# Kernel optimization log

Hardware: AMD Instinct MI355X
Metric: run time of the kernel (lower is better)

Reference implementation:

```python
import jax, jax.numpy as jnp
import numpy as np

N = 100000
D = 128       # out_feats
QK = 32       # qk_dim
E = 1600000
K_HOPS = 7    # self._k


def setup_inputs() -> dict:
    key = jax.random.key(0)
    ks = jax.random.split(key, 10)
    h_train = jax.random.normal(ks[0], (N, D), dtype=jnp.float32)
    h_ori = jax.random.normal(ks[1], (N, D), dtype=jnp.float32)
    edge_index = jax.random.randint(ks[2], (2, E), 0, N, dtype=jnp.int64)
    s = 1.0 / np.sqrt(D)
    Wq = jax.random.uniform(ks[3], (D, QK), jnp.float32, -s, s)
    bq = jnp.zeros((QK,), jnp.float32)
    Wk = jax.random.uniform(ks[4], (D, QK), jnp.float32, -s, s)
    bk = jnp.zeros((QK,), jnp.float32)
    Wv = jax.random.uniform(ks[5], (D, D), jnp.float32, -s, s)
    bv = jnp.zeros((D,), jnp.float32)
    return {"h_train": h_train, "h_ori": h_ori, "edge_index": edge_index,
            "Wq": Wq, "bq": bq, "Wk": Wk, "bk": bk, "Wv": Wv, "bv": bv}


def _propagate(x, D_invsqrt, row, col):
    h = x * D_invsqrt
    m = h[row]                                   # [E, D] gather
    out = jax.ops.segment_sum(m, col, num_segments=N)
    return out * D_invsqrt


def reference(h_train, h_ori, edge_index, Wq, bq, Wk, bk, Wv, bv):
    x = h_train
    row, col = edge_index[0], edge_index[1]
    deg = jax.ops.segment_sum(jnp.ones((E,), x.dtype), row, num_segments=N)
    deg = jnp.clip(deg, 1.0)
    D_invsqrt = (deg ** -0.5)[:, None]           # [N,1]

    a_feat = x + _propagate(x, D_invsqrt, row, col)
    stack = [a_feat]
    for _ in range(K_HOPS):
        # unnLaplacian high pass: x - Ax_hat (dropout inactive in eval)
        x = x - _propagate(x, D_invsqrt, row, col)
        stack.append(x)
    L_stack = jnp.stack(stack, axis=1)           # [N, K, D]

    # FullAttention with global mean query
    q = h_ori @ Wq + bq                          # [N, QK]
    q_global = q.mean(axis=0)                    # [QK]
    keys = L_stack @ Wk + bk                     # [N, K, QK]
    values = L_stack @ Wv + bv                   # [N, K, D]
    scale = 1.0 / np.sqrt(D)                     # D = keys input last dim
    scores = jnp.einsum('q,nkq->nk', q_global, keys) * scale
    A = jax.nn.softmax(scores, axis=-1)          # [N, K]
    V = jnp.einsum('nk,nkd->nd', A, values)      # [N, D] (== sum over K dim)
    return V
```

## Files before the change

### kernel.cpp

```cpp
#include <hip/hip_runtime.h>
#include <hip/hip_fp16.h>
#include <math.h>

#define DFEAT 128
#define QKD 32
#define NPART 512

typedef _Float16 half8 __attribute__((ext_vector_type(8)));
typedef float floatx4 __attribute__((ext_vector_type(4)));

static inline size_t align256(size_t x) { return (x + 255) & ~size_t(255); }


__global__ void count_row_kernel(const int* __restrict__ eidx, unsigned* __restrict__ cnt_row, int E) {
    int e = blockIdx.x * blockDim.x + threadIdx.x;
    if (e < E) atomicAdd(&cnt_row[eidx[e]], 1u);
}

__global__ void dinv_kernel(const unsigned* __restrict__ cnt_row, float* __restrict__ dinv,
                            float* __restrict__ dinv2, float* __restrict__ rec, int n) {
    int i = blockIdx.x * blockDim.x + threadIdx.x;
    if (i < n) {
        unsigned c = cnt_row[i];
        if (c < 1u) c = 1u;
        float fd = (float)c;
        float sq = sqrtf(fd);
        dinv[i] = 1.0f / sq;
        dinv2[i] = 1.0f / fd;
        rec[i] = sq;
    }
}


__global__ void __launch_bounds__(1024)
hist_kernel(const int* __restrict__ eidx, unsigned* __restrict__ bcount, int E, int nbuk) {
    __shared__ unsigned h[512];
    for (int i = threadIdx.x; i < 512; i += 1024) h[i] = 0;
    __syncthreads();
    int base = blockIdx.x * 8192;
    int end = base + 8192; if (end > E) end = E;
    for (int i = base + threadIdx.x; i < end; i += 1024)
        atomicAdd(&h[(unsigned)eidx[E + i] >> 8], 1u);
    __syncthreads();
    for (int i = threadIdx.x; i < nbuk; i += 1024)
        if (h[i]) atomicAdd(&bcount[i], h[i]);
}


__global__ void bscan_kernel(const unsigned* __restrict__ bcount, unsigned* __restrict__ bbase,
                             unsigned* __restrict__ bcur, unsigned* __restrict__ colptr,
                             int nbuk, int n, int E) {
    __shared__ unsigned s[512];
    int t = threadIdx.x;
    unsigned v = (t < nbuk) ? bcount[t] : 0u;
    s[t] = v; __syncthreads();
    for (int off = 1; off < 512; off <<= 1) {
        unsigned u = (t >= off) ? s[t - off] : 0u;
        __syncthreads();
        s[t] += u;
        __syncthreads();
    }
    if (t < nbuk) { unsigned e = s[t] - v; bbase[t] = e; bcur[t] = e; }
    if (t == 0) { bbase[nbuk] = (unsigned)E; colptr[n] = (unsigned)E; }
}

__global__ void __launch_bounds__(1024)
bscatter_kernel(const int* __restrict__ eidx, unsigned* __restrict__ bcur,
                unsigned* __restrict__ pairs, int E) {
    __shared__ unsigned cnt[512];
    __shared__ unsigned cur[512];
    for (int i = threadIdx.x; i < 512; i += 1024) cnt[i] = 0;
    __syncthreads();
    int base = blockIdx.x * 8192;
    int end = base + 8192; if (end > E) end = E;
    for (int i = base + threadIdx.x; i < end; i += 1024)
        atomicAdd(&cnt[(unsigned)eidx[E + i] >> 8], 1u);
    __syncthreads();
    for (int i = threadIdx.x; i < 512; i += 1024)
        cur[i] = cnt[i] ? atomicAdd(&bcur[i], cnt[i]) : 0u;
    __syncthreads();
    for (int i = base + threadIdx.x; i < end; i += 1024) {
        int col = eidx[E + i];
        int row = eidx[i];
        unsigned pos = atomicAdd(&cur[(unsigned)col >> 8], 1u);
        pairs[pos] = ((unsigned)row << 8) | (unsigned)(col & 255);
    }
}

__global__ void bsort_kernel(const unsigned* __restrict__ pairs, const unsigned* __restrict__ bbase,
                             unsigned* __restrict__ colptr, int* __restrict__ rowlist, int n) {
    __shared__ unsigned s[256];
    __shared__ unsigned cur[256];
    int b = blockIdx.x;
    unsigned beg = bbase[b], end = bbase[b + 1];
    int t = threadIdx.x;
    s[t] = 0;
    __syncthreads();
    for (unsigned i = beg + t; i < end; i += 256)
        atomicAdd(&s[pairs[i] & 255u], 1u);
    __syncthreads();
    unsigned v = s[t];
    for (int off = 1; off < 256; off <<= 1) {
        unsigned u = (t >= off) ? s[t - off] : 0u;
        __syncthreads();
        s[t] += u;
        __syncthreads();
    }
    unsigned start = beg + (s[t] - v);
    cur[t] = start;
    int c = b * 256 + t;
    if (c < n) colptr[c] = start;
    __syncthreads();
    for (unsigned i = beg + t; i < end; i += 256) {
        unsigned pk = pairs[i];
        unsigned pos = atomicAdd(&cur[pk & 255u], 1u);
        rowlist[pos] = (int)(pk >> 8);
    }
}


__global__ void scale_cvt_kernel(const float* __restrict__ h, const float* __restrict__ dinv,
                                 __half2* __restrict__ y, int n64) {
    int i = blockIdx.x * blockDim.x + threadIdx.x;
    if (i < n64) {
        float d = dinv[i >> 6];
        float2 v = reinterpret_cast<const float2*>(h)[i];
        y[i] = __floats2half2_rn(d * v.x, d * v.y);
    }
}


__global__ void cvt_wvt_kernel(const float* __restrict__ Wv, _Float16* __restrict__ wvt) {
    int t = blockIdx.x * blockDim.x + threadIdx.x;
    if (t < DFEAT * DFEAT) {
        int j = t >> 7, d = t & 127;
        wvt[t] = (_Float16)Wv[d * DFEAT + j];
    }
}


__global__ void colmean_partial_kernel(const float* __restrict__ h, float* __restrict__ partialT, int n) {
    __shared__ float s[256];
    int t = threadIdx.x;
    int col = t & 127;
    int half = t >> 7;
    float acc = 0.f;
    for (int r = blockIdx.x * 2 + half; r < n; r += gridDim.x * 2)
        acc += h[(size_t)r * DFEAT + col];
    s[t] = acc; __syncthreads();
    if (t < 128) partialT[(size_t)t * NPART + blockIdx.x] = s[t] + s[t + 128];
}

__global__ void hbar_reduce_kernel(const float* __restrict__ partialT, float* __restrict__ hbar,
                                   float inv_n) {
    __shared__ float s[256];
    int c = blockIdx.x, t = threadIdx.x;
    float acc = partialT[(size_t)c * NPART + t] + partialT[(size_t)c * NPART + t + 256];
    s[t] = acc; __syncthreads();
    for (int off = 128; off > 0; off >>= 1) {
        if (t < off) s[t] += s[t + off];
        __syncthreads();
    }
    if (t == 0) hbar[c] = s[0] * inv_n;
}

__global__ void wkq_kernel(const float* __restrict__ hbar,
                           const float* __restrict__ Wq, const float* __restrict__ bq,
                           const float* __restrict__ Wk, const float* __restrict__ bk,
                           float* __restrict__ wkq_ck) {
    __shared__ float hb[DFEAT];
    __shared__ float pq[QKD][9];
    __shared__ float qg[QKD];
    int t = threadIdx.x;
    if (t < DFEAT) hb[t] = hbar[t];
    __syncthreads();
    int q = t & 31, ch = t >> 5;
    float a = 0.f;
    int d0 = ch * 16;
#pragma unroll
    for (int d = 0; d < 16; ++d) a += hb[d0 + d] * Wq[(d0 + d) * QKD + q];
    pq[q][ch] = a;
    __syncthreads();
    if (t < QKD) {
        float s = bq[t];
#pragma unroll
        for (int c2 = 0; c2 < 8; ++c2) s += pq[t][c2];
        qg[t] = s;
    }
    __syncthreads();
    if (t < DFEAT) {
        float w = 0.f;
#pragma unroll
        for (int k = 0; k < QKD; ++k) w += Wk[t * QKD + k] * qg[k];
        wkq_ck[t] = w;
    }
    if (t == 0) {
        float c = 0.f;
        for (int k = 0; k < QKD; ++k) c += bk[k] * qg[k];
        wkq_ck[DFEAT] = c;
    }
}


__device__ __forceinline__ __half2 u2h(unsigned u) { return *reinterpret_cast<const __half2*>(&u); }

__device__ __forceinline__ void acc4(const uint2* __restrict__ yq, int r, int sl, float4& a) {
    uint2 v = yq[(size_t)r * 32 + sl];
    float2 f0 = __half22float2(u2h(v.x));
    float2 f1 = __half22float2(u2h(v.y));
    a.x += f0.x; a.y += f0.y; a.z += f1.x; a.w += f1.y;
}

__device__ __forceinline__ float hred(float s) {
    s += __shfl_xor(s, 1, 64);  s += __shfl_xor(s, 2, 64);  s += __shfl_xor(s, 4, 64);
    s += __shfl_xor(s, 8, 64);  s += __shfl_xor(s, 16, 64);
    return s;
}

__device__ __forceinline__ float4 gatherw(const uint2* __restrict__ y,
                                          const int* __restrict__ rowlist,
                                          unsigned beg, unsigned deg, unsigned mxd, int sl) {
    float4 a = make_float4(0.f, 0.f, 0.f, 0.f);
    unsigned i = 0;
    for (; i < (mxd & ~7u); i += 8) {
        unsigned rem = deg > i ? deg - i : 0;
        if (rem >= 8) {
            int4 q0 = *reinterpret_cast<const int4*>(&rowlist[beg + i]);
            int4 q1 = *reinterpret_cast<const int4*>(&rowlist[beg + i + 4]);
            uint2 v0 = y[(size_t)q0.x * 32 + sl];
            uint2 v1 = y[(size_t)q0.y * 32 + sl];
            uint2 v2 = y[(size_t)q0.z * 32 + sl];
            uint2 v3 = y[(size_t)q0.w * 32 + sl];
            uint2 v4 = y[(size_t)q1.x * 32 + sl];
            uint2 v5 = y[(size_t)q1.y * 32 + sl];
            uint2 v6 = y[(size_t)q1.z * 32 + sl];
            uint2 v7 = y[(size_t)q1.w * 32 + sl];
            __half2 sx = __hadd2(__hadd2(__hadd2(u2h(v0.x), u2h(v1.x)), __hadd2(u2h(v2.x), u2h(v3.x))),
                                 __hadd2(__hadd2(u2h(v4.x), u2h(v5.x)), __hadd2(u2h(v6.x), u2h(v7.x))));
            __half2 sy = __hadd2(__hadd2(__hadd2(u2h(v0.y), u2h(v1.y)), __hadd2(u2h(v2.y), u2h(v3.y))),
                                 __hadd2(__hadd2(u2h(v4.y), u2h(v5.y)), __hadd2(u2h(v6.y), u2h(v7.y))));
            float2 fx = __half22float2(sx), fy = __half22float2(sy);
            a.x += fx.x; a.y += fx.y; a.z += fy.x; a.w += fy.y;
        } else if (rem >= 4) {
            int4 q = *reinterpret_cast<const int4*>(&rowlist[beg + i]);
            uint2 v0 = y[(size_t)q.x * 32 + sl];
            uint2 v1 = y[(size_t)q.y * 32 + sl];
            uint2 v2 = y[(size_t)q.z * 32 + sl];
            uint2 v3 = y[(size_t)q.w * 32 + sl];
            __half2 sx = __hadd2(__hadd2(u2h(v0.x), u2h(v1.x)), __hadd2(u2h(v2.x), u2h(v3.x)));
            __half2 sy = __hadd2(__hadd2(u2h(v0.y), u2h(v1.y)), __hadd2(u2h(v2.y), u2h(v3.y)));
            float2 fx = __half22float2(sx), fy = __half22float2(sy);
            a.x += fx.x; a.y += fx.y; a.z += fy.x; a.w += fy.y;
            for (unsigned k = 4; k < rem; ++k) acc4(y, rowlist[beg + i + k], sl, a);
        } else if (rem) {
            for (unsigned k = 0; k < rem; ++k) acc4(y, rowlist[beg + i + k], sl, a);
        }
    }
    {
        unsigned rem = deg > i ? deg - i : 0;
        if (rem >= 4) {
            int4 q = *reinterpret_cast<const int4*>(&rowlist[beg + i]);
            uint2 v0 = y[(size_t)q.x * 32 + sl];
            uint2 v1 = y[(size_t)q.y * 32 + sl];
            uint2 v2 = y[(size_t)q.z * 32 + sl];
            uint2 v3 = y[(size_t)q.w * 32 + sl];
            __half2 sx = __hadd2(__hadd2(u2h(v0.x), u2h(v1.x)), __hadd2(u2h(v2.x), u2h(v3.x)));
            __half2 sy = __hadd2(__hadd2(u2h(v0.y), u2h(v1.y)), __hadd2(u2h(v2.y), u2h(v3.y)));
            float2 fx = __half22float2(sx), fy = __half22float2(sy);
            a.x += fx.x; a.y += fx.y; a.z += fy.x; a.w += fy.y;
            for (unsigned k = 4; k < rem; ++k) acc4(y, rowlist[beg + i + k], sl, a);
        } else if (rem) {
            for (unsigned k = 0; k < rem; ++k) acc4(y, rowlist[beg + i + k], sl, a);
        }
    }
    return a;
}

__device__ __forceinline__ uint2 pack4(float a, float b, float c, float d) {
    uint2 r;
    __half2 h0 = __floats2half2_rn(a, b), h1 = __floats2half2_rn(c, d);
    r.x = *reinterpret_cast<unsigned*>(&h0);
    r.y = *reinterpret_cast<unsigned*>(&h1);
    return r;
}

__global__ void __launch_bounds__(256, 8)
prop0_kernel(const uint2* __restrict__ y0,
             const int* __restrict__ rowlist, const unsigned* __restrict__ colptr,
             const float* __restrict__ dinv, const float* __restrict__ rec,
             const float* __restrict__ wkq_ck,
             uint2* __restrict__ yout, uint2* __restrict__ U,
             float* __restrict__ m_run, float* __restrict__ den_run, int n) {
    int wid = threadIdx.x >> 6, lane = threadIdx.x & 63;
    int sub = lane >> 5, sl = lane & 31;
    int c = blockIdx.x * 8 + wid * 2 + sub;
    if (c >= n) c = n - 1;
    unsigned beg = colptr[c], end = colptr[c + 1];
    unsigned deg = end - beg;
    unsigned dego = __shfl_xor(deg, 32, 64);
    unsigned mxd = deg > dego ? deg : dego;
    float4 a = gatherw(y0, rowlist, beg, deg, mxd, sl);

    float dc = dinv[c], rc = rec[c];
    size_t off = (size_t)c * 32 + sl;
    uint2 bvv = y0[off];
    float2 b0 = __half22float2(u2h(bvv.x));
    float2 b1 = __half22float2(u2h(bvv.y));
    float x0 = rc * b0.x, x1 = rc * b0.y, x2 = rc * b1.x, x3 = rc * b1.y;
    float p0 = dc * a.x, p1 = dc * a.y, p2 = dc * a.z, p3 = dc * a.w;
    float ad0 = x0 + p0, ad1 = x1 + p1, ad2 = x2 + p2, ad3 = x3 + p3;
    float sb0 = x0 - p0, sb1 = x1 - p1, sb2 = x2 - p2, sb3 = x3 - p3;
    yout[off] = pack4(dc * sb0, dc * sb1, dc * sb2, dc * sb3);

    const float scale = 0.08838834764831845f;
    float ck = wkq_ck[DFEAT];
    float4 wv = *reinterpret_cast<const float4*>(&wkq_ck[sl * 4]);
    float s0 = (hred(ad0 * wv.x + ad1 * wv.y + ad2 * wv.z + ad3 * wv.w) + ck) * scale;
    float s1 = (hred(sb0 * wv.x + sb1 * wv.y + sb2 * wv.z + sb3 * wv.w) + ck) * scale;
    float m = fmaxf(s0, s1);
    float e0 = expf(s0 - m), e1 = expf(s1 - m);
    U[off] = pack4(e0 * ad0 + e1 * sb0, e0 * ad1 + e1 * sb1,
                   e0 * ad2 + e1 * sb2, e0 * ad3 + e1 * sb3);
    if (sl == 0) { m_run[c] = m; den_run[c] = e0 + e1; }
}

__global__ void __launch_bounds__(256, 8)
prop_fused_kernel(const uint2* __restrict__ y, const int* __restrict__ rowlist,
                  const unsigned* __restrict__ colptr,
                  const float* __restrict__ dinv2, const float* __restrict__ rec,
                  const float* __restrict__ wkq_ck,
                  uint2* __restrict__ yout, uint2* __restrict__ U,
                  float* __restrict__ m_run, float* __restrict__ den_run, int n) {
    int wid = threadIdx.x >> 6, lane = threadIdx.x & 63;
    int sub = lane >> 5, sl = lane & 31;
    int c = blockIdx.x * 8 + wid * 2 + sub;
    if (c >= n) c = n - 1;
    unsigned beg = colptr[c], end = colptr[c + 1];
    unsigned deg = end - beg;
    unsigned dego = __shfl_xor(deg, 32, 64);
    unsigned mxd = deg > dego ? deg : dego;
    float4 a = gatherw(y, rowlist, beg, deg, mxd, sl);

    float d2 = dinv2[c], rc = rec[c];
    size_t off = (size_t)c * 32 + sl;
    uint2 bvv = y[off];
    float2 b0 = __half22float2(u2h(bvv.x));
    float2 b1 = __half22float2(u2h(bvv.y));
    float y0 = b0.x - d2 * a.x, y1 = b0.y - d2 * a.y;
    float y2 = b1.x - d2 * a.z, y3 = b1.y - d2 * a.w;
    yout[off] = pack4(y0, y1, y2, y3);
    float x0 = rc * y0, x1 = rc * y1, x2 = rc * y2, x3 = rc * y3;

    const float scale = 0.08838834764831845f;
    float ck = wkq_ck[DFEAT];
    float4 wv = *reinterpret_cast<const float4*>(&wkq_ck[sl * 4]);
    float s = (hred(x0 * wv.x + x1 * wv.y + x2 * wv.z + x3 * wv.w) + ck) * scale;
    float m = m_run[c], den = den_run[c];
    float m2 = fmaxf(m, s);
    float alpha = expf(m - m2), beta = expf(s - m2);
    uint2 uv = U[off];
    float2 u0 = __half22float2(u2h(uv.x));
    float2 u1 = __half22float2(u2h(uv.y));
    U[off] = pack4(u0.x * alpha + beta * x0, u0.y * alpha + beta * x1,
                   u1.x * alpha + beta * x2, u1.y * alpha + beta * x3);
    if (sl == 0) { m_run[c] = m2; den_run[c] = den * alpha + beta; }
}


__global__ void __launch_bounds__(256, 4)
final_mfma_kernel(const _Float16* __restrict__ Uh, const float* __restrict__ den,
                  const unsigned* __restrict__ wvtU, const float* __restrict__ bv,
                  float* __restrict__ out, int n) {
    __shared__ unsigned wT[8192];
    for (int i = threadIdx.x; i < 8192; i += 256) {
        int col = i >> 6, inner = i & 63;
        wT[col * 64 + (inner ^ ((col & 7) << 2))] = wvtU[i];
    }
    __syncthreads();
    int wave = threadIdx.x >> 6, lane = threadIdx.x & 63;
    int row0 = blockIdx.x * 64 + wave * 16;
    int l15 = lane & 15, grp = lane >> 4;
    int kgrp = grp * 8;
    int arow = row0 + l15; if (arow >= n) arow = n - 1;
    const _Float16* aptr = Uh + (size_t)arow * DFEAT + kgrp;
    half8 af[4];
    af[0] = *(const half8*)(aptr);
    af[1] = *(const half8*)(aptr + 32);
    af[2] = *(const half8*)(aptr + 64);
    af[3] = *(const half8*)(aptr + 96);
    const _Float16* wTh = (const _Float16*)wT;
    floatx4 acc[8];
#pragma unroll
    for (int ct = 0; ct < 8; ++ct) acc[ct] = (floatx4){0.f, 0.f, 0.f, 0.f};
#pragma unroll
    for (int kt = 0; kt < 4; ++kt) {
        int kbase = kt * 32 + kgrp;
#pragma unroll
        for (int ct = 0; ct < 8; ++ct) {
            int col = ct * 16 + l15;
            half8 bf = *(const half8*)&wTh[col * 128 + (kbase ^ ((col & 7) << 3))];
            acc[ct] = __builtin_amdgcn_mfma_f32_16x16x32_f16(af[kt], bf, acc[ct], 0, 0, 0);
        }
    }
    int m0 = row0 + grp * 4;
    float invd[4];
#pragma unroll
    for (int r = 0; r < 4; ++r) {
        int gr = m0 + r;
        invd[r] = 1.0f / den[gr < n ? gr : (n - 1)];
    }
#pragma unroll
    for (int ct = 0; ct < 8; ++ct) {
        int col = ct * 16 + l15;
        float bvc = bv[col];
#pragma unroll
        for (int r = 0; r < 4; ++r) {
            int gr = m0 + r;
            if (gr < n) out[(size_t)gr * DFEAT + col] = acc[ct][r] * invd[r] + bvc;
        }
    }
}


extern "C" void kernel_launch(void* const* d_in, const int* in_sizes, int n_in,
                              void* d_out, int out_size, void* d_ws, size_t ws_size,
                              hipStream_t stream) {
    const float* h_train = (const float*)d_in[0];
    const float* h_ori   = (const float*)d_in[1];
    const int*   eidx    = (const int*)d_in[2];
    const float* Wq = (const float*)d_in[3];
    const float* bq = (const float*)d_in[4];
    const float* Wk = (const float*)d_in[5];
    const float* bk = (const float*)d_in[6];
    const float* Wv = (const float*)d_in[7];
    const float* bv = (const float*)d_in[8];
    float* out = (float*)d_out;

    const int n = in_sizes[0] / DFEAT;
    const int E = in_sizes[2] / 2;
    const int NBUK = (n + 255) >> 8;
    const int EB = (E + 8191) / 8192;
    size_t ND2 = (size_t)n * 64;

    if (NBUK > 512) return;

    char* p = (char*)d_ws;
    auto alloc = [&](size_t bytes) { char* r = p; p += align256(bytes); return r; };
    uint2*    yA       = (uint2*)   alloc(ND2 * 4);
    uint2*    yB       = (uint2*)   alloc(ND2 * 4);
    uint2*    U16      = (uint2*)   alloc(ND2 * 4);
    int*      rowlist  = (int*)     alloc((size_t)(E + 16) * 4);
    unsigned* pairs    = (unsigned*)alloc((size_t)E * 4);
    float*    dinv     = (float*)   alloc((size_t)n * 4);
    float*    dinv2    = (float*)   alloc((size_t)n * 4);
    float*    rec      = (float*)   alloc((size_t)n * 4);
    unsigned* cnt_row  = (unsigned*)alloc((size_t)n * 4);
    unsigned* colptr   = (unsigned*)alloc((size_t)(n + 1) * 4);
    unsigned* bcount   = (unsigned*)alloc((size_t)NBUK * 4);
    unsigned* bbase    = (unsigned*)alloc((size_t)(NBUK + 1) * 4);
    unsigned* bcur     = (unsigned*)alloc((size_t)NBUK * 4);
    float*    m_run    = (float*)   alloc((size_t)n * 4);
    float*    den_run  = (float*)   alloc((size_t)n * 4);
    float*    partialT = (float*)   alloc((size_t)NPART * DFEAT * 4);
    float*    hbar     = (float*)   alloc(DFEAT * 4);
    float*    wkq_ck   = (float*)   alloc((DFEAT + 1) * 4);
    _Float16* wvt      = (_Float16*)alloc((size_t)DFEAT * DFEAT * 2);
    if ((size_t)(p - (char*)d_ws) > ws_size) return;

    hipMemsetAsync(cnt_row, 0, (size_t)n * 4, stream);
    hipMemsetAsync(bcount, 0, (size_t)NBUK * 4, stream);

    count_row_kernel<<<(E + 255) / 256, 256, 0, stream>>>(eidx, cnt_row, E);
    hist_kernel<<<EB, 1024, 0, stream>>>(eidx, bcount, E, NBUK);
    bscan_kernel<<<1, 512, 0, stream>>>(bcount, bbase, bcur, colptr, NBUK, n, E);
    bscatter_kernel<<<EB, 1024, 0, stream>>>(eidx, bcur, pairs, E);
    dinv_kernel<<<(n + 255) / 256, 256, 0, stream>>>(cnt_row, dinv, dinv2, rec, n);
    bsort_kernel<<<NBUK, 256, 0, stream>>>(pairs, bbase, colptr, rowlist, n);

    scale_cvt_kernel<<<(n * 64 + 255) / 256, 256, 0, stream>>>(h_train, dinv, (__half2*)yA, n * 64);
    cvt_wvt_kernel<<<64, 256, 0, stream>>>(Wv, wvt);

    colmean_partial_kernel<<<NPART, 256, 0, stream>>>(h_ori, partialT, n);
    hbar_reduce_kernel<<<DFEAT, 256, 0, stream>>>(partialT, hbar, 1.0f / (float)n);
    wkq_kernel<<<1, 256, 0, stream>>>(hbar, Wq, bq, Wk, bk, wkq_ck);

    prop0_kernel<<<(n + 7) / 8, 256, 0, stream>>>(yA, rowlist, colptr, dinv, rec, wkq_ck,
                                                  yB, U16, m_run, den_run, n);
    uint2* xin = yB; uint2* xout = yA;
    for (int t = 2; t <= 7; ++t) {
        prop_fused_kernel<<<(n + 7) / 8, 256, 0, stream>>>(xin, rowlist, colptr, dinv2, rec, wkq_ck,
                                                           xout, U16, m_run, den_run, n);
        uint2* tmp = xin; xin = xout; xout = tmp;
    }

    final_mfma_kernel<<<(n + 63) / 64, 256, 0, stream>>>((const _Float16*)U16, den_run,
                                                         (const unsigned*)wvt, bv, out, n);
}
```

Before: 688.0 us.

## Store all hop features and scores, defer softmax-weighted sum to final kernel

Replaces the per-hop online-softmax accumulation with a two-pass scheme. Each propagation kernel now writes its hop features into a stored fp16 stack plus a per-node score, and a new final kernel does the softmax over the 8 scores, the weighted sum over the stack and the Wv MFMA in one step. This removes the U read-modify-write and the running max/denominator state from every hop. In exchange the final kernel must re-read all 8 feature slices and the workspace grows, with a fallback to the old path if the workspace is too small. It also folds the row-degree count into the histogram kernel and runs bsort with 1024 threads per block.

```diff
diff --git a/kernel.cpp b/kernel.cpp
--- a/kernel.cpp
+++ b/kernel.cpp
@@ -11,10 +11,24 @@
 
 static inline size_t align256(size_t x) { return (x + 255) & ~size_t(255); }
 
-
-__global__ void count_row_kernel(const int* __restrict__ eidx, unsigned* __restrict__ cnt_row, int E) {
-    int e = blockIdx.x * blockDim.x + threadIdx.x;
-    if (e < E) atomicAdd(&cnt_row[eidx[e]], 1u);
+__device__ __forceinline__ __half2 u2h(unsigned u) { return *reinterpret_cast<const __half2*>(&u); }
+
+
+__global__ void __launch_bounds__(1024)
+hist_kernel(const int* __restrict__ eidx, unsigned* __restrict__ cnt_row,
+            unsigned* __restrict__ bcount, int E, int nbuk) {
+    __shared__ unsigned h[512];
+    for (int i = threadIdx.x; i < 512; i += 1024) h[i] = 0;
+    __syncthreads();
+    int base = blockIdx.x * 8192;
+    int end = base + 8192; if (end > E) end = E;
+    for (int i = base + threadIdx.x; i < end; i += 1024) {
+        atomicAdd(&cnt_row[eidx[i]], 1u);
+        atomicAdd(&h[(unsigned)eidx[E + i] >> 8], 1u);
+    }
+    __syncthreads();
+    for (int i = threadIdx.x; i < nbuk; i += 1024)
+        if (h[i]) atomicAdd(&bcount[i], h[i]);
 }
 
 __global__ void dinv_kernel(const unsigned* __restrict__ cnt_row, float* __restrict__ dinv,
@@ -29,21 +43,6 @@
         dinv2[i] = 1.0f / fd;
         rec[i] = sq;
     }
-}
-
-
-__global__ void __launch_bounds__(1024)
-hist_kernel(const int* __restrict__ eidx, unsigned* __restrict__ bcount, int E, int nbuk) {
-    __shared__ unsigned h[512];
-    for (int i = threadIdx.x; i < 512; i += 1024) h[i] = 0;
-    __syncthreads();
-    int base = blockIdx.x * 8192;
-    int end = base + 8192; if (end > E) end = E;
-    for (int i = base + threadIdx.x; i < end; i += 1024)
-        atomicAdd(&h[(unsigned)eidx[E + i] >> 8], 1u);
-    __syncthreads();
-    for (int i = threadIdx.x; i < nbuk; i += 1024)
-        if (h[i]) atomicAdd(&bcount[i], h[i]);
 }
 
 
@@ -87,31 +86,34 @@
     }
 }
 
-__global__ void bsort_kernel(const unsigned* __restrict__ pairs, const unsigned* __restrict__ bbase,
-                             unsigned* __restrict__ colptr, int* __restrict__ rowlist, int n) {
+__global__ void __launch_bounds__(1024)
+bsort_kernel(const unsigned* __restrict__ pairs, const unsigned* __restrict__ bbase,
+             unsigned* __restrict__ colptr, int* __restrict__ rowlist, int n) {
     __shared__ unsigned s[256];
     __shared__ unsigned cur[256];
     int b = blockIdx.x;
     unsigned beg = bbase[b], end = bbase[b + 1];
     int t = threadIdx.x;
-    s[t] = 0;
-    __syncthreads();
-    for (unsigned i = beg + t; i < end; i += 256)
+    if (t < 256) s[t] = 0;
+    __syncthreads();
+    for (unsigned i = beg + t; i < end; i += 1024)
         atomicAdd(&s[pairs[i] & 255u], 1u);
     __syncthreads();
-    unsigned v = s[t];
+    unsigned v = (t < 256) ? s[t] : 0u;
     for (int off = 1; off < 256; off <<= 1) {
-        unsigned u = (t >= off) ? s[t - off] : 0u;
+        unsigned u = (t < 256 && t >= off) ? s[t - off] : 0u;
         __syncthreads();
-        s[t] += u;
+        if (t < 256) s[t] += u;
         __syncthreads();
     }
-    unsigned start = beg + (s[t] - v);
-    cur[t] = start;
-    int c = b * 256 + t;
-    if (c < n) colptr[c] = start;
-    __syncthreads();
-    for (unsigned i = beg + t; i < end; i += 256) {
+    if (t < 256) {
+        unsigned start = beg + (s[t] - v);
+        cur[t] = start;
+        int c = b * 256 + t;
+        if (c < n) colptr[c] = start;
+    }
+    __syncthreads();
+    for (unsigned i = beg + t; i < end; i += 1024) {
         unsigned pk = pairs[i];
         unsigned pos = atomicAdd(&cur[pk & 255u], 1u);
         rowlist[pos] = (int)(pk >> 8);
@@ -201,8 +203,6 @@
     }
 }
 
-
-__device__ __forceinline__ __half2 u2h(unsigned u) { return *reinterpret_cast<const __half2*>(&u); }
 
 __device__ __forceinline__ void acc4(const uint2* __restrict__ yq, int r, int sl, float4& a) {
     uint2 v = yq[(size_t)r * 32 + sl];
@@ -284,6 +284,155 @@
     return r;
 }
 
+
+__global__ void __launch_bounds__(256, 8)
+prop0_st_kernel(const uint2* __restrict__ y0,
+                const int* __restrict__ rowlist, const unsigned* __restrict__ colptr,
+                const float* __restrict__ dinv, const float* __restrict__ rec,
+                const float* __restrict__ wkq_ck,
+                uint2* __restrict__ afeat_out, uint2* __restrict__ y1_out,
+                float* __restrict__ score01, int n) {
+    int wid = threadIdx.x >> 6, lane = threadIdx.x & 63;
+    int sub = lane >> 5, sl = lane & 31;
+    int c = blockIdx.x * 8 + wid * 2 + sub;
+    if (c >= n) c = n - 1;
+    unsigned beg = colptr[c], end = colptr[c + 1];
+    unsigned deg = end - beg;
+    unsigned dego = __shfl_xor(deg, 32, 64);
+    unsigned mxd = deg > dego ? deg : dego;
+    float4 a = gatherw(y0, rowlist, beg, deg, mxd, sl);
+
+    float dc = dinv[c], rc = rec[c];
+    size_t off = (size_t)c * 32 + sl;
+    uint2 bvv = y0[off];
+    float2 b0 = __half22float2(u2h(bvv.x));
+    float2 b1 = __half22float2(u2h(bvv.y));
+    float x0 = rc * b0.x, x1 = rc * b0.y, x2 = rc * b1.x, x3 = rc * b1.y;
+    float p0 = dc * a.x, p1 = dc * a.y, p2 = dc * a.z, p3 = dc * a.w;
+    float ad0 = x0 + p0, ad1 = x1 + p1, ad2 = x2 + p2, ad3 = x3 + p3;
+    float sb0 = x0 - p0, sb1 = x1 - p1, sb2 = x2 - p2, sb3 = x3 - p3;
+    afeat_out[off] = pack4(ad0, ad1, ad2, ad3);
+    y1_out[off] = pack4(dc * sb0, dc * sb1, dc * sb2, dc * sb3);
+
+    const float scale = 0.08838834764831845f;
+    float ck = wkq_ck[DFEAT];
+    float4 wv = *reinterpret_cast<const float4*>(&wkq_ck[sl * 4]);
+    float s0 = (hred(ad0 * wv.x + ad1 * wv.y + ad2 * wv.z + ad3 * wv.w) + ck) * scale;
+    float s1 = (hred(sb0 * wv.x + sb1 * wv.y + sb2 * wv.z + sb3 * wv.w) + ck) * scale;
+    if (sl == 0) { score01[c] = s0; score01[n + c] = s1; }
+}
+
+__global__ void __launch_bounds__(256, 8)
+prop_st_kernel(const uint2* __restrict__ y, const int* __restrict__ rowlist,
+               const unsigned* __restrict__ colptr,
+               const float* __restrict__ dinv2, const float* __restrict__ rec,
+               const float* __restrict__ wkq_ck,
+               uint2* __restrict__ yout, float* __restrict__ score_out, int n) {
+    int wid = threadIdx.x >> 6, lane = threadIdx.x & 63;
+    int sub = lane >> 5, sl = lane & 31;
+    int c = blockIdx.x * 8 + wid * 2 + sub;
+    if (c >= n) c = n - 1;
+    unsigned beg = colptr[c], end = colptr[c + 1];
+    unsigned deg = end - beg;
+    unsigned dego = __shfl_xor(deg, 32, 64);
+    unsigned mxd = deg > dego ? deg : dego;
+    float4 a = gatherw(y, rowlist, beg, deg, mxd, sl);
+
+    float d2 = dinv2[c], rc = rec[c];
+    size_t off = (size_t)c * 32 + sl;
+    uint2 bvv = y[off];
+    float2 b0 = __half22float2(u2h(bvv.x));
+    float2 b1 = __half22float2(u2h(bvv.y));
+    float y0 = b0.x - d2 * a.x, y1 = b0.y - d2 * a.y;
+    float y2 = b1.x - d2 * a.z, y3 = b1.y - d2 * a.w;
+    yout[off] = pack4(y0, y1, y2, y3);
+    float x0 = rc * y0, x1 = rc * y1, x2 = rc * y2, x3 = rc * y3;
+
+    const float scale = 0.08838834764831845f;
+    float ck = wkq_ck[DFEAT];
+    float4 wv = *reinterpret_cast<const float4*>(&wkq_ck[sl * 4]);
+    float s = (hred(x0 * wv.x + x1 * wv.y + x2 * wv.z + x3 * wv.w) + ck) * scale;
+    if (sl == 0) score_out[c] = s;
+}
+
+__global__ void __launch_bounds__(256, 4)
+final_stack_kernel(const _Float16* __restrict__ stack, size_t sstride,
+                   const float* __restrict__ score, const float* __restrict__ rec,
+                   const unsigned* __restrict__ wvtU, const float* __restrict__ bv,
+                   float* __restrict__ out, int n) {
+    __shared__ unsigned wT[8192];
+    for (int i = threadIdx.x; i < 8192; i += 256) {
+        int col = i >> 6, inner = i & 63;
+        wT[col * 64 + (inner ^ ((col & 7) << 2))] = wvtU[i];
+    }
+    __syncthreads();
+    int wave = threadIdx.x >> 6, lane = threadIdx.x & 63;
+    int row0 = blockIdx.x * 64 + wave * 16;
+    int l15 = lane & 15, grp = lane >> 4;
+    int kgrp = grp * 8;
+    int arow = row0 + l15; if (arow >= n) arow = n - 1;
+    float sc[8];
+#pragma unroll
+    for (int t = 0; t < 8; ++t) sc[t] = score[(size_t)t * n + arow];
+    float mx = sc[0];
+#pragma unroll
+    for (int t = 1; t < 8; ++t) mx = fmaxf(mx, sc[t]);
+    float se = 0.f;
+#pragma unroll
+    for (int t = 0; t < 8; ++t) { sc[t] = expf(sc[t] - mx); se += sc[t]; }
+    float inv = 1.0f / se;
+    float rc = rec[arow];
+    __half2 wh[8];
+#pragma unroll
+    for (int t = 0; t < 8; ++t) wh[t] = __float2half2_rn(sc[t] * inv * (t ? rc : 1.0f));
+    const _Float16* aptr = stack + (size_t)arow * DFEAT + kgrp;
+    half8 af[4];
+#pragma unroll
+    for (int kt = 0; kt < 4; ++kt) {
+        __half2 a0 = __float2half2_rn(0.f), a1 = a0, a2 = a0, a3 = a0;
+#pragma unroll
+        for (int t = 0; t < 8; ++t) {
+            uint4 v = *reinterpret_cast<const uint4*>(aptr + (size_t)t * sstride + kt * 32);
+            a0 = __hfma2(wh[t], u2h(v.x), a0);
+            a1 = __hfma2(wh[t], u2h(v.y), a1);
+            a2 = __hfma2(wh[t], u2h(v.z), a2);
+            a3 = __hfma2(wh[t], u2h(v.w), a3);
+        }
+        uint4 au;
+        au.x = *reinterpret_cast<unsigned*>(&a0);
+        au.y = *reinterpret_cast<unsigned*>(&a1);
+        au.z = *reinterpret_cast<unsigned*>(&a2);
+        au.w = *reinterpret_cast<unsigned*>(&a3);
+        af[kt] = *reinterpret_cast<half8*>(&au);
+    }
+    const _Float16* wTh = (const _Float16*)wT;
+    floatx4 acc[8];
+#pragma unroll
+    for (int ct = 0; ct < 8; ++ct) acc[ct] = (floatx4){0.f, 0.f, 0.f, 0.f};
+#pragma unroll
+    for (int kt = 0; kt < 4; ++kt) {
+        int kbase = kt * 32 + kgrp;
+#pragma unroll
+        for (int ct = 0; ct < 8; ++ct) {
+            int col = ct * 16 + l15;
+            half8 bf = *(const half8*)&wTh[col * 128 + (kbase ^ ((col & 7) << 3))];
+            acc[ct] = __builtin_amdgcn_mfma_f32_16x16x32_f16(af[kt], bf, acc[ct], 0, 0, 0);
+        }
+    }
+    int m0 = row0 + grp * 4;
+#pragma unroll
+    for (int ct = 0; ct < 8; ++ct) {
+        int col = ct * 16 + l15;
+        float bvc = bv[col];
+#pragma unroll
+        for (int r = 0; r < 4; ++r) {
+            int gr = m0 + r;
+            if (gr < n) out[(size_t)gr * DFEAT + col] = acc[ct][r] + bvc;
+        }
+    }
+}
+
+
 __global__ void __launch_bounds__(256, 8)
 prop0_kernel(const uint2* __restrict__ y0,
              const int* __restrict__ rowlist, const unsigned* __restrict__ colptr,
@@ -366,7 +515,6 @@
     if (sl == 0) { m_run[c] = m2; den_run[c] = den * alpha + beta; }
 }
 
-
 __global__ void __launch_bounds__(256, 4)
 final_mfma_kernel(const _Float16* __restrict__ Uh, const float* __restrict__ den,
                   const unsigned* __restrict__ wvtU, const float* __restrict__ bv,
@@ -440,15 +588,12 @@
     const int E = in_sizes[2] / 2;
     const int NBUK = (n + 255) >> 8;
     const int EB = (E + 8191) / 8192;
-    size_t ND2 = (size_t)n * 64;
+    size_t FB = align256((size_t)n * 256);
 
     if (NBUK > 512) return;
 
     char* p = (char*)d_ws;
     auto alloc = [&](size_t bytes) { char* r = p; p += align256(bytes); return r; };
-    uint2*    yA       = (uint2*)   alloc(ND2 * 4);
-    uint2*    yB       = (uint2*)   alloc(ND2 * 4);
-    uint2*    U16      = (uint2*)   alloc(ND2 * 4);
     int*      rowlist  = (int*)     alloc((size_t)(E + 16) * 4);
     unsigned* pairs    = (unsigned*)alloc((size_t)E * 4);
     float*    dinv     = (float*)   alloc((size_t)n * 4);
@@ -461,38 +606,63 @@
     unsigned* bcur     = (unsigned*)alloc((size_t)NBUK * 4);
     float*    m_run    = (float*)   alloc((size_t)n * 4);
     float*    den_run  = (float*)   alloc((size_t)n * 4);
+    float*    score    = (float*)   alloc((size_t)8 * n * 4);
     float*    partialT = (float*)   alloc((size_t)NPART * DFEAT * 4);
     float*    hbar     = (float*)   alloc(DFEAT * 4);
     float*    wkq_ck   = (float*)   alloc((DFEAT + 1) * 4);
     _Float16* wvt      = (_Float16*)alloc((size_t)DFEAT * DFEAT * 2);
-    if ((size_t)(p - (char*)d_ws) > ws_size) return;
+
+    size_t used = (size_t)(p - (char*)d_ws);
+    bool use_stack = (used + 9 * FB) <= ws_size;
+    uint2* y0 = nullptr; char* stack = nullptr;
+    uint2 *yA = nullptr, *yB = nullptr, *U16 = nullptr;
+    if (use_stack) {
+        y0    = (uint2*)alloc(FB);
+        stack = (char*)alloc(8 * FB);
+    } else {
+        if (used + 3 * FB > ws_size) return;
+        yA  = (uint2*)alloc(FB);
+        yB  = (uint2*)alloc(FB);
+        U16 = (uint2*)alloc(FB);
+    }
 
     hipMemsetAsync(cnt_row, 0, (size_t)n * 4, stream);
     hipMemsetAsync(bcount, 0, (size_t)NBUK * 4, stream);
 
-    count_row_kernel<<<(E + 255) / 256, 256, 0, stream>>>(eidx, cnt_row, E);
-    hist_kernel<<<EB, 1024, 0, stream>>>(eidx, bcount, E, NBUK);
+    hist_kernel<<<EB, 1024, 0, stream>>>(eidx, cnt_row, bcount, E, NBUK);
     bscan_kernel<<<1, 512, 0, stream>>>(bcount, bbase, bcur, colptr, NBUK, n, E);
     bscatter_kernel<<<EB, 1024, 0, stream>>>(eidx, bcur, pairs, E);
     dinv_kernel<<<(n + 255) / 256, 256, 0, stream>>>(cnt_row, dinv, dinv2, rec, n);
-    bsort_kernel<<<NBUK, 256, 0, stream>>>(pairs, bbase, colptr, rowlist, n);
-
-    scale_cvt_kernel<<<(n * 64 + 255) / 256, 256, 0, stream>>>(h_train, dinv, (__half2*)yA, n * 64);
+    bsort_kernel<<<NBUK, 1024, 0, stream>>>(pairs, bbase, colptr, rowlist, n);
+
     cvt_wvt_kernel<<<64, 256, 0, stream>>>(Wv, wvt);
-
     colmean_partial_kernel<<<NPART, 256, 0, stream>>>(h_ori, partialT, n);
     hbar_reduce_kernel<<<DFEAT, 256, 0, stream>>>(partialT, hbar, 1.0f / (float)n);
     wkq_kernel<<<1, 256, 0, stream>>>(hbar, Wq, bq, Wk, bk, wkq_ck);
 
-    prop0_kernel<<<(n + 7) / 8, 256, 0, stream>>>(yA, rowlist, colptr, dinv, rec, wkq_ck,
-                                                  yB, U16, m_run, den_run, n);
-    uint2* xin = yB; uint2* xout = yA;
-    for (int t = 2; t <= 7; ++t) {
-        prop_fused_kernel<<<(n + 7) / 8, 256, 0, stream>>>(xin, rowlist, colptr, dinv2, rec, wkq_ck,
-                                                           xout, U16, m_run, den_run, n);
-        uint2* tmp = xin; xin = xout; xout = tmp;
-    }
-
-    final_mfma_kernel<<<(n + 63) / 64, 256, 0, stream>>>((const _Float16*)U16, den_run,
-                                                         (const unsigned*)wvt, bv, out, n);
-}
+    int pgrid = (n + 7) / 8;
+    if (use_stack) {
+        auto slotu = [&](int t) { return (uint2*)(stack + (size_t)t * FB); };
+        scale_cvt_kernel<<<(n * 64 + 255) / 256, 256, 0, stream>>>(h_train, dinv, (__half2*)y0, n * 64);
+        prop0_st_kernel<<<pgrid, 256, 0, stream>>>(y0, rowlist, colptr, dinv, rec, wkq_ck,
+                                                   slotu(0), slotu(1), score, n);
+        for (int t = 2; t <= 7; ++t)
+            prop_st_kernel<<<pgrid, 256, 0, stream>>>(slotu(t - 1), rowlist, colptr, dinv2, rec,
+                                                      wkq_ck, slotu(t), score + (size_t)t * n, n);
+        final_stack_kernel<<<(n + 63) / 64, 256, 0, stream>>>((const _Float16*)stack, FB / 2,
+                                                              score, rec, (const unsigned*)wvt,
+                                                              bv, out, n);
+    } else {
+        scale_cvt_kernel<<<(n * 64 + 255) / 256, 256, 0, stream>>>(h_train, dinv, (__half2*)yA, n * 64);
+        prop0_kernel<<<pgrid, 256, 0, stream>>>(yA, rowlist, colptr, dinv, rec, wkq_ck,
+                                                yB, U16, m_run, den_run, n);
+        uint2* xin = yB; uint2* xout = yA;
+        for (int t = 2; t <= 7; ++t) {
+            prop_fused_kernel<<<pgrid, 256, 0, stream>>>(xin, rowlist, colptr, dinv2, rec, wkq_ck,
+                                                         xout, U16, m_run, den_run, n);
+            uint2* tmp = xin; xin = xout; xout = tmp;
+        }
+        final_mfma_kernel<<<(n + 63) / 64, 256, 0, stream>>>((const _Float16*)U16, den_run,
+                                                             (const unsigned*)wvt, bv, out, n);
+    }
+}
```

New measurement: 703.1 us. 2.2% more time.
